# Kernel optimization log

Measured on AMD Instinct MI355X. Metric: run time of the kernel, lower is better.

## Reference

```python
import jax, jax.numpy as jnp
import numpy as np

# ---- dims ----
B0, CIN, Hh, Ww = 8, 256, 96, 96
SPLIT = 8
DM = CIN // SPLIT            # 32  per-split d_model
EXPAND = 2
DIN = EXPAND * DM            # 64  d_inner
DSTATE = 64
DCONV = 3
HEADDIM = 8
NH = DIN // HEADDIM          # 8 heads
DOUT = 256
CHUNK = 32
D_IN_PROJ = 2 * DIN + 2 * DSTATE + NH  # 264
CONV_CH = DIN + 2 * DSTATE   # 192


def setup_inputs() -> dict:
    key = jax.random.key(0)
    ks = jax.random.split(key, 10)
    x = jax.random.normal(ks[0], (B0, CIN, Hh, Ww), jnp.float32)
    inp = {
        'x': x,
        'ln_w': jnp.ones((CIN,), jnp.float32),
        'ln_b': jnp.zeros((CIN,), jnp.float32),
        'skip_scale': jnp.ones((1,), jnp.float32),
        'proj_w': jax.random.normal(ks[1], (CIN, DOUT), jnp.float32) / np.sqrt(CIN),
        'proj_b': jnp.zeros((DOUT,), jnp.float32),
        'W_in': jax.random.normal(ks[2], (DM, D_IN_PROJ), jnp.float32) / np.sqrt(DM),
        'conv_w': jax.random.normal(ks[3], (CONV_CH, 1, DCONV), jnp.float32) * 0.3,
        'conv_b': jnp.zeros((CONV_CH,), jnp.float32),
        'dt_bias': jax.random.normal(ks[4], (NH,), jnp.float32) * 0.5,
        'A_log': jnp.log(jnp.arange(1.0, NH + 1.0, dtype=jnp.float32)),
        'D': jax.random.normal(ks[5], (NH,), jnp.float32) * 0.5,
        'rms_w': jnp.ones((DIN,), jnp.float32),
        'W_out': jax.random.normal(ks[6], (DIN, DM), jnp.float32) / np.sqrt(DIN),
    }
    return inp


def _layernorm(x, w, b, eps=1e-5):
    mu = jnp.mean(x, -1, keepdims=True)
    xc = x - mu
    var = jnp.mean(xc * xc, -1, keepdims=True)
    return xc * jax.lax.rsqrt(var + eps) * w + b


def _ssd(x, A, Bm, Cm, chunk):
    # x: (b,l,h,p)  A: (b,l,h)  Bm/Cm: (b,l,n); chunked SSD (Mamba2 minimal)
    b, l, h, p = x.shape
    n = Bm.shape[-1]
    nc = l // chunk
    xc = x.reshape(b, nc, chunk, h, p)
    Ac = A.reshape(b, nc, chunk, h).transpose(0, 3, 1, 2)  # (b,h,c,l)
    Bc = Bm.reshape(b, nc, chunk, n)
    Cc = Cm.reshape(b, nc, chunk, n)
    ac = jnp.cumsum(Ac, -1)                                 # (b,h,c,l)
    seg = ac[..., :, None] - ac[..., None, :]
    mask = jnp.tril(jnp.ones((chunk, chunk), bool))
    L = jnp.where(mask, jnp.exp(jnp.where(mask, seg, 0.0)), 0.0)  # (b,h,c,l,s)
    Yd = jnp.einsum('bcln,bcsn,bhcls,bcshp->bclhp', Cc, Bc, L, xc)
    decay_states = jnp.exp(ac[..., -1:] - ac)               # (b,h,c,l)
    states = jnp.einsum('bcln,bhcl,bclhp->bchpn', Bc, decay_states, xc)
    chunk_decay = jnp.exp(ac[..., -1])                      # (b,h,c)
    def step(carry, inp):
        s, d = inp
        return carry * d[..., None, None] + s, carry
    states_t = jnp.moveaxis(states, 1, 0)                   # (c,b,h,p,n)
    dec_t = jnp.moveaxis(chunk_decay, 2, 0)                 # (c,b,h)
    _, prev = jax.lax.scan(step, jnp.zeros_like(states_t[0]), (states_t, dec_t))
    prev = jnp.moveaxis(prev, 0, 1)                         # (b,c,h,p,n)
    Yo = jnp.einsum('bcln,bchpn,bhcl->bclhp', Cc, prev, jnp.exp(ac))
    return (Yd + Yo).reshape(b, l, h, p)


def _mamba2(u, W_in, conv_w, conv_b, dt_bias, A_log, D, rms_w, W_out):
    b, l, _ = u.shape
    zxbcdt = u @ W_in
    z = zxbcdt[..., :DIN]
    xBC = zxbcdt[..., DIN:DIN + CONV_CH]
    dt = jax.nn.softplus(zxbcdt[..., -NH:] + dt_bias)       # (b,l,h)
    conv = jax.lax.conv_general_dilated(
        xBC.transpose(0, 2, 1), conv_w, (1,), [(DCONV - 1, 0)],
        dimension_numbers=('NCH', 'OIH', 'NCH'), feature_group_count=CONV_CH)
    xBC = jax.nn.silu(conv + conv_b[None, :, None]).transpose(0, 2, 1)
    xs = xBC[..., :DIN].reshape(b, l, NH, HEADDIM)
    Bm = xBC[..., DIN:DIN + DSTATE]
    Cm = xBC[..., DIN + DSTATE:]
    A = -jnp.exp(A_log)
    y = _ssd(xs * dt[..., None], dt * A, Bm, Cm, CHUNK)
    y = y + xs * D[None, None, :, None]
    y = y.reshape(b, l, DIN) * jax.nn.silu(z)               # gated
    y = y * jax.lax.rsqrt(jnp.mean(y * y, -1, keepdims=True) + 1e-5) * rms_w
    return y @ W_out


def reference(x, ln_w, ln_b, skip_scale, proj_w, proj_b, W_in, conv_w, conv_b,
              dt_bias, A_log, D, rms_w, W_out):
    Bn, C, h, w = x.shape
    L = h * w
    xf = x.reshape(Bn, C, L).transpose(0, 2, 1)             # (B,L,C)
    xn = _layernorm(xf, ln_w, ln_b)
    d = C // SPLIT
    xs = jnp.moveaxis(xn.reshape(Bn, L, SPLIT, d), 2, 0)    # (S,B,L,d)
    xs = xs.reshape(SPLIT * Bn, L, d)
    ym = _mamba2(xs, W_in, conv_w, conv_b, dt_bias, A_log, D, rms_w, W_out)
    ym = ym + skip_scale * xs
    ym = jnp.moveaxis(ym.reshape(SPLIT, Bn, L, d), 0, 2).reshape(Bn, L, C)
    ym = _layernorm(ym, ln_w, ln_b)
    out = ym @ proj_w + proj_b                              # (B,L,DOUT)
    return out.transpose(0, 2, 1).reshape(Bn, DOUT, h, w)
```

## Files before the change

### kernel.cpp

```cpp
#include <hip/hip_runtime.h>
#include <hip/hip_fp16.h>
#include <math.h>

typedef unsigned short u16;
typedef unsigned int u32;
typedef _Float16 half2_t __attribute__((ext_vector_type(2)));
typedef _Float16 f16x8 __attribute__((ext_vector_type(8)));
typedef float f32x4 __attribute__((ext_vector_type(4)));

#define B0N 8
#define LSEQ 9216
#define NSEQ 64
#define NCHUNK 288
#define DM 32
#define DPROJ 264
#define CONVCH 192
#define XC4 208
#define URH 40
#define CHH 204
#define ZBS 66
#define C2H 132
#define TTS 40
#define GS 36
#define YH5 264

#ifndef __has_builtin
#define __has_builtin(x) 0
#endif

__device__ __forceinline__ float silu_(float v) { return v / (1.f + __expf(-v)); }

__global__ __launch_bounds__(256) void k1_ln_split(const float* __restrict__ x,
                                                   const float* __restrict__ lnw,
                                                   const float* __restrict__ lnb,
                                                   __half* __restrict__ u) {
  __shared__ float tile[256 * 33];
  __shared__ float mu[32], rs[32], wv[256], bv[256];
  __shared__ float ps[32 * 9], ps2[32 * 9];
  const int b = blockIdx.y, l0 = blockIdx.x * 32, t = threadIdx.x;
  wv[t] = lnw[t];
  bv[t] = lnb[t];
#pragma unroll 4
  for (int i = 0; i < 32; ++i) {
    int c = i * 8 + (t >> 5), ll = t & 31;
    tile[c * 33 + ll] = x[((size_t)b * 256 + c) * LSEQ + l0 + ll];
  }
  __syncthreads();
  {
    const int ll = t & 31, seg = t >> 5;
    float s = 0.f, s2 = 0.f;
#pragma unroll 8
    for (int i = 0; i < 32; ++i) {
      float v = tile[(seg * 32 + i) * 33 + ll];
      s += v; s2 += v * v;
    }
    ps[ll * 9 + seg] = s;
    ps2[ll * 9 + seg] = s2;
  }
  __syncthreads();
  if (t < 32) {
    float s = 0.f, s2 = 0.f;
#pragma unroll
    for (int seg = 0; seg < 8; ++seg) { s += ps[t * 9 + seg]; s2 += ps2[t * 9 + seg]; }
    float m = s * (1.f / 256.f);
    mu[t] = m;
    rs[t] = rsqrtf(s2 * (1.f / 256.f) - m * m + 1e-5f);
  }
  __syncthreads();
#pragma unroll 4
  for (int i = 0; i < 32; ++i) {
    int sp = i >> 2, sub = i & 3;
    int ll = sub * 8 + (t >> 5), dm = t & 31;
    int c = sp * 32 + dm;
    float v = (tile[c * 33 + ll] - mu[ll]) * rs[ll] * wv[c] + bv[c];
    u[(((size_t)(sp * B0N + b)) * LSEQ + l0 + ll) * DM + dm] = __float2half(v);
  }
}

__global__ __launch_bounds__(256, 5) void k2_states(
    const __half* __restrict__ u, const float* __restrict__ Win,
    const float* __restrict__ convw, const float* __restrict__ convb,
    const float* __restrict__ dtbias, const float* __restrict__ Alog,
    __half* __restrict__ S, float* __restrict__ cdec) {
  __shared__ __align__(16) char smem[32512];
  _Float16* ur_h = (_Float16*)smem;
  _Float16* CH2h = (_Float16*)(smem + 3840);
  _Float16* Ah   = (_Float16*)(smem + 3840);
  __half*   Sout = (__half*)(smem + 8960);
  _Float16* xst  = (_Float16*)(smem + 18176);
  _Float16* Bt   = (_Float16*)(smem + 23296);
  float* dtraw = (float*)(smem + 28416);
  float* dtv   = (float*)(smem + 29440);
  float* acs   = (float*)(smem + 30464);
  float* wv2   = (float*)(smem + 31488);
  const int c = blockIdx.x, sq = blockIdx.y, t = threadIdx.x;
  const int l0 = c * 32;
  const int lane = t & 63, wvi = t >> 6, g = lane >> 4, c16 = lane & 15;
  const size_t ubase = (size_t)sq * (LSEQ * DM);
  const f32x4 zero4 = {0.f, 0.f, 0.f, 0.f};

  for (int idx = t; idx < 48 * 32; idx += 256) {
    int r = idx >> 5, dm = idx & 31;
    int l = l0 - 2 + r;
    _Float16 v = (_Float16)0.f;
    if (r < 34 && l >= 0) v = ((const _Float16*)u)[ubase + (size_t)l * DM + dm];
    ur_h[r * URH + dm] = v;
  }
  f16x8 bfr[2];
#pragma unroll
  for (int i = 0; i < 2; ++i) {
    int col = 64 + (wvi + i * 4) * 16 + c16;
#pragma unroll
    for (int j = 0; j < 8; ++j) bfr[i][j] = (_Float16)Win[(g * 8 + j) * DPROJ + col];
  }
  __syncthreads();

  {
    f16x8 am[3];
#pragma unroll
    for (int mt = 0; mt < 3; ++mt)
      am[mt] = *(const f16x8*)&ur_h[(mt * 16 + c16) * URH + g * 8];
#pragma unroll
    for (int i = 0; i < 2; ++i) {
      int colc = (wvi + i * 4) * 16 + c16;
#pragma unroll
      for (int mt = 0; mt < 3; ++mt) {
        f32x4 acc = __builtin_amdgcn_mfma_f32_16x16x32_f16(am[mt], bfr[i], zero4, 0, 0, 0);
#pragma unroll
        for (int r = 0; r < 4; ++r) {
          int R = mt * 16 + 4 * g + r;
          if (R < 34) CH2h[R * C2H + colc] = (_Float16)acc[r];
        }
      }
    }
  }
  __syncthreads();

  {
    const int ch0 = t & 63, lbq = t >> 6;
#pragma unroll
    for (int cr = 0; cr < 2; ++cr) {
      int ch = ch0 + cr * 64;
      float w0 = convw[ch * 3 + 0], w1 = convw[ch * 3 + 1], w2 = convw[ch * 3 + 2];
      float cb = convb[ch];
      float a = (float)CH2h[(lbq * 8 + 0) * C2H + ch];
      float b = (float)CH2h[(lbq * 8 + 1) * C2H + ch];
      f16x8 out;
#pragma unroll
      for (int j = 0; j < 8; ++j) {
        float cn = (float)CH2h[(lbq * 8 + j + 2) * C2H + ch];
        out[j] = (_Float16)silu_(a * w0 + b * w1 + cn * w2 + cb);
        a = b; b = cn;
      }
      if (cr == 0) *(f16x8*)&xst[ch0 * TTS + lbq * 8] = out;
      else         *(f16x8*)&Bt[ch0 * TTS + lbq * 8] = out;
    }
    int l = t >> 3, h = t & 7;
    float raw = 0.f;
#pragma unroll
    for (int dm = 0; dm < 32; ++dm)
      raw += (float)ur_h[(l + 2) * URH + dm] * Win[dm * DPROJ + 256 + h];
    dtraw[l * 8 + h] = raw;
  }
  __syncthreads();

  {
    const int l = t & 31, h = t >> 5;
    float raw = dtraw[l * 8 + h] + dtbias[h];
    float dt = (raw > 20.f) ? raw : log1pf(__expf(raw));
    float x = dt;
#pragma unroll
    for (int d = 1; d < 32; d <<= 1) {
      float y = __shfl_up(x, d, 32);
      if (l >= d) x += y;
    }
    const float A = -__expf(Alog[h]);
    dtv[t] = dt;
    acs[t] = A * x;
    if (l == 31) cdec[(sq * NCHUNK + c) * 8 + h] = __expf(A * x);
  }
  __syncthreads();

  {
    int h = t >> 5;
    wv2[t] = __expf(acs[h * 32 + 31] - acs[t]) * dtv[t];
  }
  __syncthreads();
  {
    const int hp = t >> 2, lb2 = (t & 3) * 8;
    const float* w = &wv2[(hp >> 3) * 32 + lb2];
    const _Float16* xr = &xst[hp * TTS + lb2];
    f16x8 ov;
#pragma unroll
    for (int i = 0; i < 8; ++i) ov[i] = (_Float16)((float)xr[i] * w[i]);
    *(f16x8*)&Ah[hp * TTS + lb2] = ov;
  }
  __syncthreads();

  {
    const int mt = wvi;
    f16x8 aS = *(const f16x8*)&Ah[(mt * 16 + c16) * TTS + g * 8];
#pragma unroll
    for (int nt = 0; nt < 4; ++nt) {
      f16x8 bS = *(const f16x8*)&Bt[(nt * 16 + c16) * TTS + g * 8];
      f32x4 acc = __builtin_amdgcn_mfma_f32_16x16x32_f16(aS, bS, zero4, 0, 0, 0);
#pragma unroll
      for (int r = 0; r < 4; ++r)
        Sout[(mt * 16 + 4 * g + r) * 72 + nt * 16 + c16] = __float2half(acc[r]);
    }
  }
  __syncthreads();
  const size_t sbase = (size_t)(sq * NCHUNK + c) * 4096;
#pragma unroll
  for (int i = 0; i < 2; ++i) {
    int idx = i * 256 + t;
    int hp = idx >> 3, part = idx & 7;
    *(uint4*)(S + sbase + hp * 64 + part * 8) = *(const uint4*)&Sout[hp * 72 + part * 8];
  }
}

__global__ __launch_bounds__(128) void k3_scan(__half* __restrict__ S,
                                               const float* __restrict__ cdec) {
  __shared__ float cd[NCHUNK];
  const int sq = blockIdx.x >> 3, h = blockIdx.x & 7, t = threadIdx.x;
  for (int i = t; i < NCHUNK; i += 128) cd[i] = cdec[(sq * NCHUNK + i) * 8 + h];
  __syncthreads();
  __half* p = S + (size_t)sq * NCHUNK * 4096 + h * 512 + t * 4;
  uint2 f0 = *(const uint2*)(p);
  uint2 f1 = *(const uint2*)(p + 4096);
  uint2 f2 = *(const uint2*)(p + 2 * 4096);
  uint2 f3 = *(const uint2*)(p + 3 * 4096);
  float car0 = 0.f, car1 = 0.f, car2 = 0.f, car3 = 0.f;
  for (int c = 0; c < NCHUNK; c += 4) {
#define K3_STEP(F, K)                                                              \
    {                                                                              \
      half2_t lo = *(half2_t*)&F.x, hi = *(half2_t*)&F.y;                          \
      float s0 = (float)lo.x, s1 = (float)lo.y, s2 = (float)hi.x, s3 = (float)hi.y;\
      int nc = c + K + 4; if (nc > NCHUNK - 1) nc = NCHUNK - 1;                    \
      F = *(const uint2*)(p + (size_t)nc * 4096);                                  \
      half2_t olo, ohi;                                                            \
      olo.x = (_Float16)car0; olo.y = (_Float16)car1;                              \
      ohi.x = (_Float16)car2; ohi.y = (_Float16)car3;                              \
      uint2 ov; ov.x = *(u32*)&olo; ov.y = *(u32*)&ohi;                            \
      *(uint2*)(p + (size_t)(c + K) * 4096) = ov;                                  \
      float d = cd[c + K];                                                         \
      car0 = car0 * d + s0; car1 = car1 * d + s1;                                  \
      car2 = car2 * d + s2; car3 = car3 * d + s3;                                  \
    }
    K3_STEP(f0, 0)
    K3_STEP(f1, 1)
    K3_STEP(f2, 2)
    K3_STEP(f3, 3)
#undef K3_STEP
  }
}

__global__ __launch_bounds__(256, 4) void k4_out(
    const __half* __restrict__ u, const float* __restrict__ Win,
    const float* __restrict__ convw, const float* __restrict__ convb,
    const float* __restrict__ dtbias, const float* __restrict__ Alog,
    const float* __restrict__ Dp, const float* __restrict__ rmsw,
    const float* __restrict__ Wout, const float* __restrict__ skip,
    const __half* __restrict__ S, __half* __restrict__ ym) {
  __shared__ __align__(16) _Float16 ur_h[48 * URH];
  __shared__ __align__(16) _Float16 CHh[34 * CHH];
  __shared__ __align__(16) __half xch[32 * XC4];
  __shared__ __align__(16) float dtraw[256];
  __shared__ __align__(16) float dtv[256], acs[256];
  __shared__ __align__(16) _Float16 zbuf[32 * ZBS];
  const int c = blockIdx.x, sq = blockIdx.y, t = threadIdx.x;
  const int l0 = c * 32;
  const int lane = t & 63, wvi = t >> 6, g = lane >> 4, c16 = lane & 15;
  const size_t ubase = (size_t)sq * (LSEQ * DM);
  const f32x4 zero4 = {0.f, 0.f, 0.f, 0.f};

  const size_t sbase = (size_t)(sq * NCHUNK + c) * 4096;
  uint4 sv0, sv1;
  {
    const uint4* sp = (const uint4*)(S + sbase);
    sv0 = sp[t * 2];
    sv1 = sp[t * 2 + 1];
  }
  for (int idx = t; idx < 48 * 32; idx += 256) {
    int r = idx >> 5, dm = idx & 31;
    int l = l0 - 2 + r;
    _Float16 v = (_Float16)0.f;
    if (r < 34 && l >= 0) v = ((const _Float16*)u)[ubase + (size_t)l * DM + dm];
    ur_h[r * URH + dm] = v;
  }
  f16x8 bfr[3];
#pragma unroll
  for (int i = 0; i < 3; ++i) {
    int col = 64 + (wvi + i * 4) * 16 + c16;
#pragma unroll
    for (int j = 0; j < 8; ++j) bfr[i][j] = (_Float16)Win[(g * 8 + j) * DPROJ + col];
  }
  f16x8 bz;
  {
    int col = wvi * 16 + c16;
#pragma unroll
    for (int j = 0; j < 8; ++j) bz[j] = (_Float16)Win[(g * 8 + j) * DPROJ + col];
  }
  __syncthreads();

  {
    f16x8 am[3];
#pragma unroll
    for (int mt = 0; mt < 3; ++mt)
      am[mt] = *(const f16x8*)&ur_h[(mt * 16 + c16) * URH + g * 8];
#pragma unroll
    for (int i = 0; i < 3; ++i) {
      int colc = (wvi + i * 4) * 16 + c16;
#pragma unroll
      for (int mt = 0; mt < 3; ++mt) {
        f32x4 acc = __builtin_amdgcn_mfma_f32_16x16x32_f16(am[mt], bfr[i], zero4, 0, 0, 0);
#pragma unroll
        for (int r = 0; r < 4; ++r) {
          int R = mt * 16 + 4 * g + r;
          if (R < 34) CHh[R * CHH + colc] = (_Float16)acc[r];
        }
      }
    }
#pragma unroll
    for (int mz = 0; mz < 2; ++mz) {
      f16x8 az = *(const f16x8*)&ur_h[(2 + mz * 16 + c16) * URH + g * 8];
      f32x4 acc = __builtin_amdgcn_mfma_f32_16x16x32_f16(az, bz, zero4, 0, 0, 0);
#pragma unroll
      for (int r = 0; r < 4; ++r) {
        int lY = mz * 16 + 4 * g + r;
        zbuf[lY * ZBS + wvi * 16 + c16] = (_Float16)acc[r];
      }
    }
  }
  __syncthreads();

  {
    const int ch0 = t & 63, lbq = t >> 6;
#pragma unroll
    for (int cr = 0; cr < 3; ++cr) {
      int ch = ch0 + cr * 64;
      float w0 = convw[ch * 3 + 0], w1 = convw[ch * 3 + 1], w2 = convw[ch * 3 + 2];
      float cb = convb[ch];
      float a = (float)CHh[(lbq * 8 + 0) * CHH + ch];
      float b = (float)CHh[(lbq * 8 + 1) * CHH + ch];
#pragma unroll
      for (int j = 0; j < 8; ++j) {
        float cn = (float)CHh[(lbq * 8 + j + 2) * CHH + ch];
        float v = a * w0 + b * w1 + cn * w2 + cb;
        xch[(lbq * 8 + j) * XC4 + ch] = __float2half(silu_(v));
        a = b; b = cn;
      }
    }
    int l = t >> 3, h = t & 7;
    float raw = 0.f;
#pragma unroll
    for (int dm = 0; dm < 32; ++dm)
      raw += (float)ur_h[(l + 2) * URH + dm] * Win[dm * DPROJ + 256 + h];
    dtraw[l * 8 + h] = raw;
  }
  __syncthreads();

  {
    char* pvb = (char*)CHh;
    int hp = t >> 2, part = t & 3;
    *(uint4*)(pvb + hp * 144 + part * 32) = sv0;
    *(uint4*)(pvb + hp * 144 + part * 32 + 16) = sv1;
  }
  {
    const int l = t & 31, h = t >> 5;
    float raw = dtraw[l * 8 + h] + dtbias[h];
    float dt = (raw > 20.f) ? raw : log1pf(__expf(raw));
    float x = dt;
#pragma unroll
    for (int d = 1; d < 32; d <<= 1) {
      float y = __shfl_up(x, d, 32);
      if (l >= d) x += y;
    }
    dtv[t] = dt;
    acs[t] = -__expf(Alog[h]) * x;
  }
  __syncthreads();

  float* Gm = (float*)((char*)CHh + 9216);
  {
    float ev = __expf(acs[t]);
    dtraw[t] = ev;
    const int mt = wvi >> 1, nt = wvi & 1;
    f32x4 acc = zero4;
#pragma unroll
    for (int kk = 0; kk < 2; ++kk) {
      f16x8 aC = *(const f16x8*)&xch[(mt * 16 + c16) * XC4 + 128 + kk * 32 + g * 8];
      f16x8 bB = *(const f16x8*)&xch[(nt * 16 + c16) * XC4 + 64 + kk * 32 + g * 8];
      acc = __builtin_amdgcn_mfma_f32_16x16x32_f16(aC, bB, acc, 0, 0, 0);
    }
#pragma unroll
    for (int r = 0; r < 4; ++r)
      Gm[(mt * 16 + 4 * g + r) * GS + nt * 16 + c16] = acc[r];
  }
  __syncthreads();

  {
    const int s2b = g * 8;
    float gv[2][8];
#pragma unroll
    for (int mt = 0; mt < 2; ++mt) {
      const float* gr = &Gm[(mt * 16 + c16) * GS + s2b];
      float4 g0 = *(const float4*)gr;
      float4 g1 = *(const float4*)(gr + 4);
      gv[mt][0] = g0.x; gv[mt][1] = g0.y; gv[mt][2] = g0.z; gv[mt][3] = g0.w;
      gv[mt][4] = g1.x; gv[mt][5] = g1.y; gv[mt][6] = g1.z; gv[mt][7] = g1.w;
    }
#pragma unroll
    for (int hh = 0; hh < 2; ++hh) {
      const int h = 2 * wvi + hh;
      const float* ap = &acs[h * 32 + s2b];
      const float* dp = &dtv[h * 32 + s2b];
      float4 a0 = *(const float4*)ap, a1 = *(const float4*)(ap + 4);
      float4 d0 = *(const float4*)dp, d1 = *(const float4*)(dp + 4);
      const float av[8] = {a0.x, a0.y, a0.z, a0.w, a1.x, a1.y, a1.z, a1.w};
      const float dv[8] = {d0.x, d0.y, d0.z, d0.w, d1.x, d1.y, d1.z, d1.w};
      f16x8 bfr2;
#pragma unroll
      for (int j = 0; j < 8; ++j)
        bfr2[j] = *(const _Float16*)&xch[(s2b + j) * XC4 + h * 8 + (c16 & 7)];
#pragma unroll
      for (int mt = 0; mt < 2; ++mt) {
        const int row = mt * 16 + c16;
        const float arow = acs[h * 32 + row];
        f16x8 afr;
#pragma unroll
        for (int j = 0; j < 8; ++j) {
          float m = gv[mt][j] * __expf(arow - av[j]) * dv[j];
          afr[j] = (_Float16)((s2b + j <= row) ? m : 0.f);
        }
        f32x4 dacc = __builtin_amdgcn_mfma_f32_16x16x32_f16(afr, bfr2, zero4, 0, 0, 0);
        if (c16 < 8) {
#pragma unroll
          for (int r = 0; r < 4; ++r)
            xch[(mt * 16 + 4 * g + r) * XC4 + 64 + h * 8 + c16] = __float2half(dacc[r]);
        }
      }
    }
  }
  __syncthreads();

  {
    const __half* pvh = (const __half*)CHh;
#pragma unroll
    for (int mt = 0; mt < 2; ++mt) {
      f32x4 acc = zero4;
#pragma unroll
      for (int kk = 0; kk < 2; ++kk) {
        f16x8 aC = *(const f16x8*)&xch[(mt * 16 + c16) * XC4 + 128 + kk * 32 + g * 8];
        f16x8 bP = *(const f16x8*)&pvh[(wvi * 16 + c16) * 72 + kk * 32 + g * 8];
        acc = __builtin_amdgcn_mfma_f32_16x16x32_f16(aC, bP, acc, 0, 0, 0);
      }
      int hp = wvi * 16 + c16;
#pragma unroll
      for (int r = 0; r < 4; ++r) {
        int l = mt * 16 + 4 * g + r;
        float e = dtraw[(hp >> 3) * 32 + l];
        __half* yb = &xch[l * XC4 + 64 + hp];
        *yb = __float2half(__half2float(*yb) + acc[r] * e);
      }
    }
  }
  __syncthreads();

  {
    const int hp = t & 63;
    const float dcoef = Dp[hp >> 3];
#pragma unroll
    for (int k = 0; k < 8; ++k) {
      int l = (k * 256 + t) >> 6;
      float y = __half2float(xch[l * XC4 + 64 + hp]) + (float)xch[l * XC4 + hp] * dcoef;
      float z = (float)zbuf[l * ZBS + hp];
      y *= z / (1.f + __expf(-z));
      xch[l * XC4 + 64 + hp] = __float2half(y);
    }
  }
  __syncthreads();

  float* rp = Gm;
  float* scl = (float*)ur_h;
  {
    const int l = t & 31, seg = t >> 5;
    float p = 0.f;
#pragma unroll
    for (int k = 0; k < 8; ++k) {
      float v = __half2float(xch[l * XC4 + 64 + seg * 8 + k]);
      p += v * v;
    }
    rp[l * 9 + seg] = p;
  }
  __syncthreads();
  if (t < 32) {
    float s2s = 0.f;
#pragma unroll
    for (int seg = 0; seg < 8; ++seg) s2s += rp[t * 9 + seg];
    scl[t] = rsqrtf(s2s * (1.f / 64.f) + 1e-5f);
  }
  __syncthreads();

  for (int idx = t; idx < 2048; idx += 256) {
    int l = idx >> 6, hp = idx & 63;
    xch[l * XC4 + 64 + hp] =
        __float2half(__half2float(xch[l * XC4 + 64 + hp]) * scl[l] * rmsw[hp]);
  }
  __syncthreads();

  {
    const float skipv = skip[0];
    const int mt = wvi >> 1, nt = wvi & 1;
    f32x4 acc = zero4;
#pragma unroll
    for (int kk = 0; kk < 2; ++kk) {
      f16x8 aY = *(const f16x8*)&xch[(mt * 16 + c16) * XC4 + 64 + kk * 32 + g * 8];
      f16x8 bW;
#pragma unroll
      for (int j = 0; j < 8; ++j)
        bW[j] = (_Float16)Wout[(kk * 32 + g * 8 + j) * 32 + nt * 16 + c16];
      acc = __builtin_amdgcn_mfma_f32_16x16x32_f16(aY, bW, acc, 0, 0, 0);
    }
#pragma unroll
    for (int r = 0; r < 4; ++r) {
      int l = mt * 16 + 4 * g + r;
      int dm = nt * 16 + c16;
      size_t gi = ubase + (size_t)(l0 + l) * DM + dm;
      ym[gi] = __float2half(acc[r] + skipv * __half2float(u[gi]));
    }
  }
}

__global__ __launch_bounds__(256, 4) void k5_ln_proj(const __half* __restrict__ ym,
                                                     const float* __restrict__ lnw,
                                                     const float* __restrict__ lnb,
                                                     const float* __restrict__ pw,
                                                     const float* __restrict__ pb,
                                                     float* __restrict__ outp) {
  __shared__ __align__(16) char buf[33792];
  __shared__ float mu[32], rs[32], wv[256], bv[256];
  __shared__ float ps[32 * 9], ps2[32 * 9];
  _Float16* yh = (_Float16*)buf;
  float* res = (float*)buf;
  const int b = blockIdx.y, l0 = blockIdx.x * 32, t = threadIdx.x;
  const int lane = t & 63, wvi = t >> 6, g = lane >> 4, c16 = lane & 15;
  const f32x4 zero4 = {0.f, 0.f, 0.f, 0.f};
  wv[t] = lnw[t];
  bv[t] = lnb[t];
  for (int sp = 0; sp < 8; ++sp) {
#pragma unroll
    for (int i = 0; i < 2; ++i) {
      int idx = i * 256 + t;
      int ll = idx >> 4, dmp = (idx & 15) * 2;
      u32 v = *(const u32*)&ym[(((size_t)(sp * B0N + b)) * LSEQ + l0 + ll) * DM + dmp];
      *(u32*)&yh[ll * YH5 + sp * 32 + dmp] = v;
    }
  }
  __syncthreads();
  {
    const int ll = t & 31, seg = t >> 5;
    float s = 0.f, s2 = 0.f;
#pragma unroll 8
    for (int i = 0; i < 32; ++i) {
      float v = (float)yh[ll * YH5 + seg * 32 + i];
      s += v; s2 += v * v;
    }
    ps[ll * 9 + seg] = s;
    ps2[ll * 9 + seg] = s2;
  }
  __syncthreads();
  if (t < 32) {
    float s = 0.f, s2 = 0.f;
#pragma unroll
    for (int seg = 0; seg < 8; ++seg) { s += ps[t * 9 + seg]; s2 += ps2[t * 9 + seg]; }
    float m = s * (1.f / 256.f);
    mu[t] = m;
    rs[t] = rsqrtf(s2 * (1.f / 256.f) - m * m + 1e-5f);
  }
  __syncthreads();
#pragma unroll
  for (int i = 0; i < 32; ++i) {
    int idx = i * 256 + t;
    int ll = idx >> 8, ch = idx & 255;
    float v = ((float)yh[ll * YH5 + ch] - mu[ll]) * rs[ll] * wv[ch] + bv[ch];
    yh[ll * YH5 + ch] = (_Float16)v;
  }
  __syncthreads();
  f16x8 am[16];
#pragma unroll
  for (int mt = 0; mt < 2; ++mt)
#pragma unroll
    for (int kk = 0; kk < 8; ++kk)
      am[mt * 8 + kk] = *(const f16x8*)&yh[(mt * 16 + c16) * YH5 + kk * 32 + g * 8];
  __syncthreads();
#pragma unroll
  for (int ni = 0; ni < 4; ++ni) {
    const int col = (wvi + ni * 4) * 16 + c16;
    f32x4 acc0 = zero4, acc1 = zero4;
#pragma unroll
    for (int kk = 0; kk < 8; ++kk) {
      f16x8 bW;
#pragma unroll
      for (int j = 0; j < 8; ++j)
        bW[j] = (_Float16)pw[(size_t)(kk * 32 + g * 8 + j) * 256 + col];
      acc0 = __builtin_amdgcn_mfma_f32_16x16x32_f16(am[kk], bW, acc0, 0, 0, 0);
      acc1 = __builtin_amdgcn_mfma_f32_16x16x32_f16(am[8 + kk], bW, acc1, 0, 0, 0);
    }
    const float bias = pb[col];
#pragma unroll
    for (int r = 0; r < 4; ++r) {
      res[col * 33 + 4 * g + r] = acc0[r] + bias;
      res[col * 33 + 16 + 4 * g + r] = acc1[r] + bias;
    }
  }
  __syncthreads();
  for (int idx = t; idx < 8192; idx += 256) {
    int o = idx >> 5, l = idx & 31;
    outp[((size_t)(b * 256 + o)) * LSEQ + l0 + l] = res[o * 33 + l];
  }
}

extern "C" void kernel_launch(void* const* d_in, const int* in_sizes, int n_in,
                              void* d_out, int out_size, void* d_ws, size_t ws_size,
                              hipStream_t stream) {
  (void)in_sizes; (void)n_in; (void)out_size;
  const float* x     = (const float*)d_in[0];
  const float* lnw   = (const float*)d_in[1];
  const float* lnb   = (const float*)d_in[2];
  const float* skip  = (const float*)d_in[3];
  const float* pw    = (const float*)d_in[4];
  const float* pb    = (const float*)d_in[5];
  const float* Win   = (const float*)d_in[6];
  const float* convw = (const float*)d_in[7];
  const float* convb = (const float*)d_in[8];
  const float* dtb   = (const float*)d_in[9];
  const float* Alog  = (const float*)d_in[10];
  const float* Dp    = (const float*)d_in[11];
  const float* rmsw  = (const float*)d_in[12];
  const float* Wout  = (const float*)d_in[13];
  float* outp = (float*)d_out;

  const size_t NEED = 227082240ull;
  if (ws_size < NEED) return;
  char* ws = (char*)d_ws;
  __half* u    = (__half*)ws;
  __half* S    = (__half*)(ws + 37748736);
  float*  cdec = (float*)(ws + 188743680);
  __half* ym   = (__half*)(ws + 189333504);

  k1_ln_split<<<dim3(288, 8), 256, 0, stream>>>(x, lnw, lnb, u);
  k2_states<<<dim3(288, 64), 256, 0, stream>>>(u, Win, convw, convb, dtb, Alog, S, cdec);
  k3_scan<<<dim3(512), 128, 0, stream>>>(S, cdec);
  k4_out<<<dim3(288, 64), 256, 0, stream>>>(u, Win, convw, convb, dtb, Alog, Dp, rmsw,
                                            Wout, skip, S, ym);
  k5_ln_proj<<<dim3(288, 8), 256, 0, stream>>>(ym, lnw, lnb, pw, pb, outp);
}
```

Baseline: 638.3 us.

## Vectorize LN loads, widen scan parallelism, and relax k2 occupancy bound

The first LayerNorm kernel now loads its input as float4 instead of scalar floats, and the final LN/projection kernel loads ym rows as 16-byte uint4 vectors. The scan kernel doubles its threads per block, so each thread carries two state elements instead of four, with an 8-deep prefetch in place of 4-deep, to expose more parallelism on the serial chunk recurrence. The k2 launch bound is lowered from 5 to 4 waves per SIMD, giving the compiler more registers. The float4 stores into the padded 33-stride LDS tile may cause bank conflicts, and k2 may lose occupancy.

```diff
diff --git a/kernel.cpp b/kernel.cpp
--- a/kernel.cpp
+++ b/kernel.cpp
@@ -40,10 +40,15 @@
   const int b = blockIdx.y, l0 = blockIdx.x * 32, t = threadIdx.x;
   wv[t] = lnw[t];
   bv[t] = lnb[t];
-#pragma unroll 4
-  for (int i = 0; i < 32; ++i) {
-    int c = i * 8 + (t >> 5), ll = t & 31;
-    tile[c * 33 + ll] = x[((size_t)b * 256 + c) * LSEQ + l0 + ll];
+#pragma unroll
+  for (int i = 0; i < 8; ++i) {
+    int idx = i * 256 + t;
+    int cc = idx >> 3, part = idx & 7;
+    float4 v = *(const float4*)&x[((size_t)b * 256 + cc) * LSEQ + l0 + part * 4];
+    tile[cc * 33 + part * 4 + 0] = v.x;
+    tile[cc * 33 + part * 4 + 1] = v.y;
+    tile[cc * 33 + part * 4 + 2] = v.z;
+    tile[cc * 33 + part * 4 + 3] = v.w;
   }
   __syncthreads();
   {
@@ -77,7 +82,7 @@
   }
 }
 
-__global__ __launch_bounds__(256, 5) void k2_states(
+__global__ __launch_bounds__(256, 4) void k2_states(
     const __half* __restrict__ u, const float* __restrict__ Win,
     const float* __restrict__ convw, const float* __restrict__ convb,
     const float* __restrict__ dtbias, const float* __restrict__ Alog,
@@ -219,38 +224,42 @@
   }
 }
 
-__global__ __launch_bounds__(128) void k3_scan(__half* __restrict__ S,
+__global__ __launch_bounds__(256) void k3_scan(__half* __restrict__ S,
                                                const float* __restrict__ cdec) {
   __shared__ float cd[NCHUNK];
   const int sq = blockIdx.x >> 3, h = blockIdx.x & 7, t = threadIdx.x;
-  for (int i = t; i < NCHUNK; i += 128) cd[i] = cdec[(sq * NCHUNK + i) * 8 + h];
-  __syncthreads();
-  __half* p = S + (size_t)sq * NCHUNK * 4096 + h * 512 + t * 4;
-  uint2 f0 = *(const uint2*)(p);
-  uint2 f1 = *(const uint2*)(p + 4096);
-  uint2 f2 = *(const uint2*)(p + 2 * 4096);
-  uint2 f3 = *(const uint2*)(p + 3 * 4096);
-  float car0 = 0.f, car1 = 0.f, car2 = 0.f, car3 = 0.f;
-  for (int c = 0; c < NCHUNK; c += 4) {
-#define K3_STEP(F, K)                                                              \
-    {                                                                              \
-      half2_t lo = *(half2_t*)&F.x, hi = *(half2_t*)&F.y;                          \
-      float s0 = (float)lo.x, s1 = (float)lo.y, s2 = (float)hi.x, s3 = (float)hi.y;\
-      int nc = c + K + 4; if (nc > NCHUNK - 1) nc = NCHUNK - 1;                    \
-      F = *(const uint2*)(p + (size_t)nc * 4096);                                  \
-      half2_t olo, ohi;                                                            \
-      olo.x = (_Float16)car0; olo.y = (_Float16)car1;                              \
-      ohi.x = (_Float16)car2; ohi.y = (_Float16)car3;                              \
-      uint2 ov; ov.x = *(u32*)&olo; ov.y = *(u32*)&ohi;                            \
-      *(uint2*)(p + (size_t)(c + K) * 4096) = ov;                                  \
-      float d = cd[c + K];                                                         \
-      car0 = car0 * d + s0; car1 = car1 * d + s1;                                  \
-      car2 = car2 * d + s2; car3 = car3 * d + s3;                                  \
+  for (int i = t; i < NCHUNK; i += 256) cd[i] = cdec[(sq * NCHUNK + i) * 8 + h];
+  __syncthreads();
+  __half* p = S + (size_t)sq * NCHUNK * 4096 + h * 512 + t * 2;
+  u32 f0 = *(const u32*)(p);
+  u32 f1 = *(const u32*)(p + 4096);
+  u32 f2 = *(const u32*)(p + 2 * 4096);
+  u32 f3 = *(const u32*)(p + 3 * 4096);
+  u32 f4 = *(const u32*)(p + 4 * 4096);
+  u32 f5 = *(const u32*)(p + 5 * 4096);
+  u32 f6 = *(const u32*)(p + 6 * 4096);
+  u32 f7 = *(const u32*)(p + 7 * 4096);
+  float car0 = 0.f, car1 = 0.f;
+  for (int c = 0; c < NCHUNK; c += 8) {
+#define K3_STEP(F, K)                                                    \
+    {                                                                    \
+      half2_t s2h = *(half2_t*)&F;                                       \
+      float s0 = (float)s2h.x, s1 = (float)s2h.y;                        \
+      int nc = c + K + 8; if (nc > NCHUNK - 1) nc = NCHUNK - 1;          \
+      F = *(const u32*)(p + (size_t)nc * 4096);                          \
+      half2_t o; o.x = (_Float16)car0; o.y = (_Float16)car1;             \
+      *(u32*)(p + (size_t)(c + K) * 4096) = *(u32*)&o;                   \
+      float d = cd[c + K];                                               \
+      car0 = car0 * d + s0; car1 = car1 * d + s1;                        \
     }
     K3_STEP(f0, 0)
     K3_STEP(f1, 1)
     K3_STEP(f2, 2)
     K3_STEP(f3, 3)
+    K3_STEP(f4, 4)
+    K3_STEP(f5, 5)
+    K3_STEP(f6, 6)
+    K3_STEP(f7, 7)
 #undef K3_STEP
   }
 }
@@ -548,14 +557,12 @@
   const f32x4 zero4 = {0.f, 0.f, 0.f, 0.f};
   wv[t] = lnw[t];
   bv[t] = lnb[t];
-  for (int sp = 0; sp < 8; ++sp) {
-#pragma unroll
-    for (int i = 0; i < 2; ++i) {
-      int idx = i * 256 + t;
-      int ll = idx >> 4, dmp = (idx & 15) * 2;
-      u32 v = *(const u32*)&ym[(((size_t)(sp * B0N + b)) * LSEQ + l0 + ll) * DM + dmp];
-      *(u32*)&yh[ll * YH5 + sp * 32 + dmp] = v;
-    }
+#pragma unroll
+  for (int i = 0; i < 4; ++i) {
+    int idx = i * 256 + t;
+    int sp = idx >> 7, rem = idx & 127, ll = rem >> 2, part = rem & 3;
+    uint4 v = *(const uint4*)&ym[(((size_t)(sp * B0N + b)) * LSEQ + l0 + ll) * DM + part * 8];
+    *(uint4*)&yh[ll * YH5 + sp * 32 + part * 8] = v;
   }
   __syncthreads();
   {
@@ -651,7 +658,7 @@
 
   k1_ln_split<<<dim3(288, 8), 256, 0, stream>>>(x, lnw, lnb, u);
   k2_states<<<dim3(288, 64), 256, 0, stream>>>(u, Win, convw, convb, dtb, Alog, S, cdec);
-  k3_scan<<<dim3(512), 128, 0, stream>>>(S, cdec);
+  k3_scan<<<dim3(512), 256, 0, stream>>>(S, cdec);
   k4_out<<<dim3(288, 64), 256, 0, stream>>>(u, Win, convw, convb, dtb, Alog, Dp, rmsw,
                                             Wout, skip, S, ym);
   k5_ln_proj<<<dim3(288, 8), 256, 0, stream>>>(ym, lnw, lnb, pw, pb, outp);
```

Result: no change. 631.0 us (-1.2%).
